# Kernel tuning notes

Hardware: AMD Instinct MI355X
Metric: run time of the kernel (lower is better)

The kernel has to match this reference:

```python
import jax, jax.numpy as jnp
import numpy as np


def _temporal_gated_conv(x, W, b):
    """x: (B,T,N,C) -> (B,T-Kt+1,N,Co). W: (1,Kt,C,2*Co), b: (2*Co,).
    Matches torch Conv2d(in,2*out,(1,Kt)) over (B,C,N,T) followed by GLU."""
    xh = x.transpose(0, 2, 1, 3)  # (B,N,T,C) as NHWC, kernel (1,Kt) over (N,T)
    y = jax.lax.conv_general_dilated(
        xh, W, window_strides=(1, 1), padding='VALID',
        dimension_numbers=('NHWC', 'HWIO', 'NHWC')) + b  # (B,N,T',2Co)
    lhs, rhs = jnp.split(y, 2, axis=-1)
    y = lhs * jax.nn.sigmoid(rhs)
    return y.transpose(0, 2, 1, 3)  # (B,T',N,Co)


def _spatial_graph_conv(x, cheb, Theta):
    """x: (B,T,N,C), cheb: (K,N,N), Theta: (K,C,Co).
    Faithful to torch code: step_x is CUMULATIVELY multiplied by T_k."""
    K = cheb.shape[0]
    cur = x
    acc = jnp.zeros(x.shape[:3] + (Theta.shape[-1],), dtype=x.dtype)
    for k in range(K):  # K is small and structural
        cur = jnp.einsum('mn,btnc->btmc', cheb[k], cur)
        acc = acc + jnp.einsum('btnc,co->btno', cur, Theta[k])
    return jax.nn.relu(acc)


def setup_inputs() -> dict:
    key = jax.random.key(0)
    ks = jax.random.split(key, 7)
    B, T, N, C = 16, 64, 1024, 2
    Kt, Kc, temporal_dim, spatial_dim = 3, 3, 64, 16
    s = 0.05
    return {
        'x': jax.random.normal(ks[0], (B, T, N, C), jnp.float32),
        'cheb': jax.random.normal(ks[1], (Kc, N, N), jnp.float32) * (1.0 / np.sqrt(N)),
        'W1': jax.random.normal(ks[2], (1, Kt, C, 2 * temporal_dim), jnp.float32) * s,
        'b1': jax.random.normal(ks[3], (2 * temporal_dim,), jnp.float32) * s,
        'Theta': jax.random.normal(ks[4], (Kc, temporal_dim, spatial_dim), jnp.float32) * s,
        'W2': jax.random.normal(ks[5], (1, Kt, spatial_dim, 2 * temporal_dim), jnp.float32) * s,
        'b2': jax.random.normal(ks[6], (2 * temporal_dim,), jnp.float32) * s,
    }


def reference(x, cheb, W1, b1, Theta, W2, b2):
    h = _temporal_gated_conv(x, W1, b1)          # (B, T-Kt+1, N, temporal_dim)
    h = _spatial_graph_conv(h, cheb, Theta)      # (B, T-Kt+1, N, spatial_dim)
    out = _temporal_gated_conv(h, W2, b2)        # (B, T-2*(Kt-1), N, temporal_dim)
    return out
```

## Files before the change

### kernel.cpp

```cpp
#include <hip/hip_runtime.h>
#include <stdint.h>

typedef __attribute__((ext_vector_type(8))) short bf16x8;
typedef __attribute__((ext_vector_type(4))) float f32x4;

__device__ __forceinline__ unsigned short f2bf(float f) {
  union { float f; unsigned u; } v; v.f = f;
  unsigned r = v.u + 0x7FFFu + ((v.u >> 16) & 1u);
  return (unsigned short)(r >> 16);
}

__device__ __forceinline__ float sigm(float x) { return 1.0f / (1.0f + __expf(-x)); }

__device__ __forceinline__ void gload16(const void* g, void* l) {
  __builtin_amdgcn_global_load_lds((const __attribute__((address_space(1))) void*)g,
                                   (__attribute__((address_space(3))) void*)l, 16, 0, 0);
}

__device__ __forceinline__ void bar() {
  __builtin_amdgcn_sched_barrier(0);
  __builtin_amdgcn_s_barrier();
  __builtin_amdgcn_sched_barrier(0);
}

__global__ void k0_prep(const float* __restrict__ cheb, unsigned short* __restrict__ cb1,
                        unsigned short* __restrict__ cb2, unsigned short* __restrict__ Pbig) {
  int i = blockIdx.x * blockDim.x + threadIdx.x;
  unsigned short h = f2bf(cheb[i]);
  int which = i >> 20, r = i & 1048575;
  if (which == 0) Pbig[(size_t)(r >> 10) * 3072 + (r & 1023)] = h;
  else if (which == 1) cb1[r] = h;
  else cb2[r] = h;
}

__global__ void tposebf(const unsigned short* __restrict__ s1, int ss1, unsigned short* __restrict__ d1,
                        const unsigned short* __restrict__ s2, int ss2, unsigned short* __restrict__ d2) {
  const unsigned short* src = blockIdx.z ? s2 : s1;
  unsigned short* dst = blockIdx.z ? d2 : d1;
  const int ss = blockIdx.z ? ss2 : ss1;
  __shared__ unsigned short t[64][65];
  const int c = threadIdx.x & 63, r4 = threadIdx.x >> 6;
  const int r0 = blockIdx.y * 64, c0 = blockIdx.x * 64;
#pragma unroll
  for (int r = 0; r < 64; r += 4) t[r + r4][c] = src[(size_t)(r0 + r + r4) * ss + c0 + c];
  __syncthreads();
#pragma unroll
  for (int r = 0; r < 64; r += 4) dst[(size_t)(c0 + r + r4) * 1024 + r0 + c] = t[c][r + r4];
}

__global__ __launch_bounds__(256) void gemm_bt(
    const unsigned short* __restrict__ A, const unsigned short* __restrict__ Bt,
    unsigned short* __restrict__ C, int K, int ldc, int coloff,
    const unsigned short* __restrict__ A2, const unsigned short* __restrict__ Bt2,
    unsigned short* __restrict__ C2, int ldc2, int coloff2) {
  __shared__ __align__(16) unsigned short sA[128 * 32];
  __shared__ __align__(16) unsigned short sB[128 * 32];
  const unsigned short* Ap = A;
  const unsigned short* Bp = Bt;
  unsigned short* Cp = C;
  int ld = ldc, co = coloff;
  if (blockIdx.z) { Ap = A2; Bp = Bt2; Cp = C2; ld = ldc2; co = coloff2; }
  const int mb = blockIdx.x, nb = blockIdx.y;
  const int tid = threadIdx.x;
  const int lane = tid & 63;
  const int w = tid >> 6;
  const int m0 = mb * 128, n0 = nb * 128;
  const int wm = (w >> 1) * 64, wn = (w & 1) * 64;
  const int lr = lane & 15, lg = lane >> 4;
  const f32x4 ZV = {0.f, 0.f, 0.f, 0.f};
  f32x4 acc[4][4];
#pragma unroll
  for (int f = 0; f < 4; ++f)
#pragma unroll
    for (int g = 0; g < 4; ++g) acc[f][g] = ZV;
  const int r2 = tid >> 2, kp = tid & 3;
  const size_t rowA0 = (size_t)(m0 + r2) * K;
  const size_t rowA1 = (size_t)(m0 + 64 + r2) * K;
  const size_t rowB0 = (size_t)(n0 + r2) * K;
  const size_t rowB1 = (size_t)(n0 + 64 + r2) * K;
  unsigned short* la = &sA[w * 512];
  unsigned short* lb = &sB[w * 512];
  for (int k0 = 0; k0 < K; k0 += 32) {
    const int kc = k0 + kp * 8;
    gload16(Ap + rowA0 + kc, la);
    gload16(Ap + rowA1 + kc, la + 2048);
    gload16(Bp + rowB0 + kc, lb);
    gload16(Bp + rowB1 + kc, lb + 2048);
    __syncthreads();
    bf16x8 av[4], bv[4];
#pragma unroll
    for (int f = 0; f < 4; ++f)
      av[f] = *(const bf16x8*)&sA[(wm + f * 16 + lr) * 32 + lg * 8];
#pragma unroll
    for (int g = 0; g < 4; ++g)
      bv[g] = *(const bf16x8*)&sB[(wn + g * 16 + lr) * 32 + lg * 8];
#pragma unroll
    for (int f = 0; f < 4; ++f)
#pragma unroll
      for (int g = 0; g < 4; ++g)
        acc[f][g] = __builtin_amdgcn_mfma_f32_16x16x32_bf16(av[f], bv[g], acc[f][g], 0, 0, 0);
    __syncthreads();
  }
#pragma unroll
  for (int f = 0; f < 4; ++f) {
    const int m = m0 + wm + f * 16 + lg * 4;
#pragma unroll
    for (int g = 0; g < 4; ++g) {
      const int col = co + n0 + wn + g * 16 + lr;
#pragma unroll
      for (int i = 0; i < 4; ++i)
        Cp[(size_t)(m + i) * ld + col] = f2bf(acc[f][g][i]);
    }
  }
}

__device__ __forceinline__ void dec_chunk(int s, int& row, int& c) {
  const int r3 = (((s >> 2) ^ (s >> 4)) & 1) | (((s >> 3) & 1) << 1) | (((s >> 4) & 1) << 2);
  const int u = s ^ r3;
  row = u >> 2;
  c = u & 3;
}

__global__ __launch_bounds__(512, 1) void gemm_big(
    const unsigned short* __restrict__ A, const unsigned short* __restrict__ Bt,
    unsigned short* __restrict__ C) {
  constexpr int K = 3072, NT = 96;
  __shared__ __align__(16) unsigned short lds[3 * 16384];
  const int tid = threadIdx.x;
  const int lane = tid & 63, w = tid >> 6;
  const int wr = w >> 2, wc = w & 3;
  const int lr = lane & 15, lg = lane >> 4;
  const int lin = blockIdx.x;
  const int v = (lin & 7) * 31 + (lin >> 3);
  const int mb = v & 3, nb = v >> 2;
  const int m0 = mb * 256, n0 = nb * 256;

  int r0_, c0_, r1_, c1_;
  dec_chunk((w * 2 + 0) * 64 + lane, r0_, c0_);
  dec_chunk((w * 2 + 1) * 64 + lane, r1_, c1_);
  const unsigned short* sA0 = A + (size_t)(m0 + r0_) * K + c0_ * 8;
  const unsigned short* sA1 = A + (size_t)(m0 + r1_) * K + c1_ * 8;
  const unsigned short* sB0 = Bt + (size_t)(n0 + r0_) * K + c0_ * 8;
  const unsigned short* sB1 = Bt + (size_t)(n0 + r1_) * K + c1_ * 8;
  const int ldsoff0 = (w * 2 + 0) * 512, ldsoff1 = (w * 2 + 1) * 512;

  f32x4 acc[8][4];
  const f32x4 ZV = {0.f, 0.f, 0.f, 0.f};
#pragma unroll
  for (int f = 0; f < 8; ++f)
#pragma unroll
    for (int g = 0; g < 4; ++g) acc[f][g] = ZV;

  const int aoff = (((wr * 128 + lr) * 64 + lg * 16) ^ ((lr & 7) << 4));
  const int boff = (((wc * 64 + lr) * 64 + lg * 16) ^ ((lr & 7) << 4));

#define STAGE(T, BUF)                                          \
  do {                                                         \
    unsigned short* ba_ = lds + (BUF) * 16384;                 \
    const int k0_ = (T) * 32;                                  \
    gload16(sA0 + k0_, ba_ + ldsoff0);                         \
    gload16(sA1 + k0_, ba_ + ldsoff1);                         \
    gload16(sB0 + k0_, ba_ + 8192 + ldsoff0);                  \
    gload16(sB1 + k0_, ba_ + 8192 + ldsoff1);                  \
  } while (0)

  STAGE(0, 0);
  STAGE(1, 1);
  STAGE(2, 2);
  asm volatile("s_waitcnt vmcnt(8)" ::: "memory");
  bar();

  int cur = 0;
  for (int t = 0; t < NT; ++t) {
    {
      const char* ba = (const char*)(lds + cur * 16384);
      const char* bb = ba + 16384;
      bf16x8 av[8], bv[4];
#pragma unroll
      for (int f = 0; f < 8; ++f)
        av[f] = *(const bf16x8*)(ba + aoff + f * 1024);
#pragma unroll
      for (int g = 0; g < 4; ++g)
        bv[g] = *(const bf16x8*)(bb + boff + g * 1024);
      __builtin_amdgcn_s_setprio(1);
#pragma unroll
      for (int f = 0; f < 8; ++f)
#pragma unroll
        for (int g = 0; g < 4; ++g)
          acc[f][g] = __builtin_amdgcn_mfma_f32_16x16x32_bf16(av[f], bv[g], acc[f][g], 0, 0, 0);
      __builtin_amdgcn_s_setprio(0);
    }
    bar();
    if (t + 3 < NT) STAGE(t + 3, cur);
    if (t <= NT - 4) {
      asm volatile("s_waitcnt vmcnt(8)" ::: "memory");
    } else if (t == NT - 3) {
      asm volatile("s_waitcnt vmcnt(4)" ::: "memory");
    } else if (t == NT - 2) {
      asm volatile("s_waitcnt vmcnt(0)" ::: "memory");
    }
    bar();
    cur = (cur == 2) ? 0 : cur + 1;
  }
#undef STAGE

#pragma unroll
  for (int g = 0; g < 4; ++g) {
    const int n = n0 + wc * 64 + g * 16;
    const size_t jb = (size_t)(n >> 4) * 16384;
#pragma unroll
    for (int f = 0; f < 8; ++f) {
      const int m = m0 + wr * 128 + f * 16 + lg * 4;
#pragma unroll
      for (int i = 0; i < 4; ++i)
        C[jb + (size_t)(m + i) * 16 + lr] = f2bf(fmaxf(acc[f][g][i], 0.f));
    }
  }
}

__global__ __launch_bounds__(256) void k1_fused(
    const float* __restrict__ x, const float* __restrict__ W1, const float* __restrict__ b1,
    const float* __restrict__ Theta, unsigned short* __restrict__ Zt) {
  __shared__ __align__(16) unsigned short hs[4 * 64 * 68];
  __shared__ __align__(16) unsigned short th[3 * 16 * 72];
  __shared__ __align__(16) unsigned short tr[64 * 68];
  const int tid = threadIdx.x, lane = tid & 63, w = tid >> 6;
  const int n0 = blockIdx.x * 64;
  const int bt0 = blockIdx.y * 4;
  const int bt = bt0 + w;
  const int b = bt / 62, t = bt - b * 62;
  float xv[6];
#pragma unroll
  for (int kt = 0; kt < 3; ++kt) {
    const float2 p = *(const float2*)&x[(size_t)((b * 64 + t + kt) * 1024 + n0 + lane) * 2];
    xv[kt * 2] = p.x;
    xv[kt * 2 + 1] = p.y;
  }
  float h[64];
#pragma unroll
  for (int ch = 0; ch < 64; ++ch) {
    float l = b1[ch], r = b1[64 + ch];
#pragma unroll
    for (int q = 0; q < 6; ++q) {
      l += xv[q] * W1[q * 128 + ch];
      r += xv[q] * W1[q * 128 + 64 + ch];
    }
    h[ch] = l * sigm(r);
  }
#pragma unroll
  for (int c8 = 0; c8 < 8; ++c8) {
    union { unsigned short u[8]; uint4 v; } pk;
#pragma unroll
    for (int j = 0; j < 8; ++j) pk.u[j] = f2bf(h[c8 * 8 + j]);
    *(uint4*)&hs[(w * 64 + lane) * 68 + c8 * 8] = pk.v;
  }
  for (int idx = tid; idx < 3072; idx += 256) {
    const int kc = idx >> 10, o = (idx >> 6) & 15, c = idx & 63;
    th[kc * 1152 + o * 72 + c] = f2bf(Theta[((kc << 6) | c) * 16 + o]);
  }
  __syncthreads();
  const int lr = lane & 15, lg = lane >> 4;
  const f32x4 ZV = {0.f, 0.f, 0.f, 0.f};
  for (int kc = 0; kc < 3; ++kc) {
    const bf16x8 av0 = *(const bf16x8*)&th[kc * 1152 + lr * 72 + lg * 8];
    const bf16x8 av1 = *(const bf16x8*)&th[kc * 1152 + lr * 72 + 32 + lg * 8];
    f32x4 acc[4];
#pragma unroll
    for (int ns = 0; ns < 4; ++ns) acc[ns] = ZV;
#pragma unroll
    for (int ns = 0; ns < 4; ++ns) {
      const bf16x8 bv0 = *(const bf16x8*)&hs[(w * 64 + ns * 16 + lr) * 68 + lg * 8];
      const bf16x8 bv1 = *(const bf16x8*)&hs[(w * 64 + ns * 16 + lr) * 68 + 32 + lg * 8];
      acc[ns] = __builtin_amdgcn_mfma_f32_16x16x32_bf16(av0, bv0, acc[ns], 0, 0, 0);
      acc[ns] = __builtin_amdgcn_mfma_f32_16x16x32_bf16(av1, bv1, acc[ns], 0, 0, 0);
    }
    if (kc) __syncthreads();
#pragma unroll
    for (int ns = 0; ns < 4; ++ns)
#pragma unroll
      for (int i = 0; i < 4; ++i)
        tr[(w * 16 + lg * 4 + i) * 68 + ns * 16 + lr] = f2bf(acc[ns][i]);
    __syncthreads();
#pragma unroll
    for (int rd = 0; rd < 2; ++rd) {
      const int cidx = rd * 256 + tid;
      const int rl = cidx >> 3, ck = cidx & 7;
      const uint4 v = *(const uint4*)&tr[rl * 68 + ck * 8];
      *(uint4*)&Zt[(size_t)(bt0 * 16 + rl) * 3072 + kc * 1024 + n0 + ck * 8] = v;
    }
  }
}

__global__ __launch_bounds__(256) void k3_out(
    const unsigned short* __restrict__ accb, const float* __restrict__ W2,
    const float* __restrict__ b2, float* __restrict__ out) {
  __shared__ __align__(16) unsigned short sW[128 * 72];
  const int tid = threadIdx.x, lane = tid & 63, w = tid >> 6;
  const int lr = lane & 15, lg = lane >> 4;
  const int n0 = blockIdx.x * 256;
  const int btp = blockIdx.y;
  const int b = btp / 60, tt = btp - b * 60;
  for (int idx = tid; idx < 2048; idx += 256) {
    const int ch = idx >> 4, k = 48 + (idx & 15);
    sW[ch * 72 + k] = 0;
  }
  for (int idx = tid; idx < 6144; idx += 256) {
    const int k = idx >> 7, ch = idx & 127;
    sW[ch * 72 + k] = f2bf(W2[idx]);
  }
  const int rowb = n0 + w * 64;
  const bf16x8 ZB = {0, 0, 0, 0, 0, 0, 0, 0};
  bf16x8 av[4][2];
#pragma unroll
  for (int f = 0; f < 4; ++f)
#pragma unroll
    for (int hh = 0; hh < 2; ++hh) {
      const int gk = hh * 32 + lg * 8;
      const int kt = gk >> 4, ci = gk & 15;
      av[f][hh] = ZB;
      if (kt < 3)
        av[f][hh] = *(const bf16x8*)&accb[(size_t)(b * 62 + tt + kt) * 16384 +
                                          (size_t)(rowb + f * 16 + lr) * 16 + ci];
    }
  __syncthreads();
  const size_t obase = (size_t)(b * 60 + tt) * 65536;
  const f32x4 ZV = {0.f, 0.f, 0.f, 0.f};
#pragma unroll
  for (int gl = 0; gl < 4; ++gl) {
    const int chl = gl * 16 + lr;
    const bf16x8 bl0 = *(const bf16x8*)&sW[chl * 72 + lg * 8];
    const bf16x8 bl1 = *(const bf16x8*)&sW[chl * 72 + 32 + lg * 8];
    const bf16x8 br0 = *(const bf16x8*)&sW[(64 + chl) * 72 + lg * 8];
    const bf16x8 br1 = *(const bf16x8*)&sW[(64 + chl) * 72 + 32 + lg * 8];
    f32x4 aL[4], aR[4];
#pragma unroll
    for (int f = 0; f < 4; ++f) { aL[f] = ZV; aR[f] = ZV; }
#pragma unroll
    for (int f = 0; f < 4; ++f) {
      aL[f] = __builtin_amdgcn_mfma_f32_16x16x32_bf16(av[f][0], bl0, aL[f], 0, 0, 0);
      aL[f] = __builtin_amdgcn_mfma_f32_16x16x32_bf16(av[f][1], bl1, aL[f], 0, 0, 0);
      aR[f] = __builtin_amdgcn_mfma_f32_16x16x32_bf16(av[f][0], br0, aR[f], 0, 0, 0);
      aR[f] = __builtin_amdgcn_mfma_f32_16x16x32_bf16(av[f][1], br1, aR[f], 0, 0, 0);
    }
    const float bbl = b2[chl], bbr = b2[64 + chl];
#pragma unroll
    for (int f = 0; f < 4; ++f)
#pragma unroll
      for (int i = 0; i < 4; ++i) {
        const float pl = aL[f][i] + bbl;
        const float pr = aR[f][i] + bbr;
        out[obase + (size_t)(rowb + f * 16 + lg * 4 + i) * 64 + chl] = pl * sigm(pr);
      }
  }
}

extern "C" void kernel_launch(void* const* d_in, const int* in_sizes, int n_in,
                              void* d_out, int out_size, void* d_ws, size_t ws_size,
                              hipStream_t stream) {
  const float* x    = (const float*)d_in[0];
  const float* cheb = (const float*)d_in[1];
  const float* W1   = (const float*)d_in[2];
  const float* b1   = (const float*)d_in[3];
  const float* Th   = (const float*)d_in[4];
  const float* W2   = (const float*)d_in[5];
  const float* b2   = (const float*)d_in[6];
  float* out = (float*)d_out;

  char* ws = (char*)d_ws;
  const size_t MB = 1u << 20;
  unsigned short* cb1  = (unsigned short*)(ws);
  unsigned short* cb2  = (unsigned short*)(ws + 2 * MB);
  unsigned short* Pbig = (unsigned short*)(ws + 4 * MB);
  unsigned short* t0   = (unsigned short*)(ws + 10 * MB);
  unsigned short* t1   = (unsigned short*)(ws + 12 * MB);
  unsigned short* Qb   = (unsigned short*)(ws + 14 * MB);
  unsigned short* accb = (unsigned short*)(ws + 14 * MB);
  unsigned short* Zt   = (unsigned short*)d_out;

  k0_prep<<<12288, 256, 0, stream>>>(cheb, cb1, cb2, Pbig);
  tposebf<<<dim3(16, 16, 2), 256, 0, stream>>>(Pbig, 3072, t0, cb1, 1024, t1);
  gemm_bt<<<dim3(8, 8, 2), 256, 0, stream>>>(cb1, t0, Pbig, 1024, 3072, 1024,
                                             cb2, t1, Qb, 1024, 0);
  gemm_bt<<<dim3(8, 8, 1), 256, 0, stream>>>(Qb, t0, Pbig, 1024, 3072, 2048,
                                             cb1, t0, Pbig, 1024, 0);
  k1_fused<<<dim3(16, 248), 256, 0, stream>>>(x, W1, b1, Th, Zt);
  gemm_big<<<dim3(248), dim3(512), 0, stream>>>(Pbig, Zt, accb);
  k3_out<<<dim3(4, 960), 256, 0, stream>>>(accb, W2, b2, out);
}
```

Before: 304.0 us.

## Software-pipeline LDS reads with register double-buffering and four-stage global prefetch

Restructures the big GEMM main loop so the LDS fragment reads for the next K-step are issued before the MFMA block of the current step, using two register buffers and a loop unrolled by two. The LDS ring grows from three to four stages, giving one more prefetch in flight. The intent is to hide LDS read latency behind the MFMAs and cut the stall before each barrier. The cost is higher register pressure from the doubled fragments and 128KB of LDS per block. The launch-bounds hint of two blocks per CU likely cannot be met with that much LDS and may just constrain register allocation.

```diff
diff --git a/kernel.cpp b/kernel.cpp
--- a/kernel.cpp
+++ b/kernel.cpp
@@ -121,11 +121,11 @@
   c = u & 3;
 }
 
-__global__ __launch_bounds__(512, 1) void gemm_big(
+__global__ __launch_bounds__(512, 2) void gemm_big(
     const unsigned short* __restrict__ A, const unsigned short* __restrict__ Bt,
     unsigned short* __restrict__ C) {
   constexpr int K = 3072, NT = 96;
-  __shared__ __align__(16) unsigned short lds[3 * 16384];
+  __shared__ __align__(16) unsigned short lds[4 * 16384];
   const int tid = threadIdx.x;
   const int lane = tid & 63, w = tid >> 6;
   const int wr = w >> 2, wc = w & 3;
@@ -154,9 +154,11 @@
   const int aoff = (((wr * 128 + lr) * 64 + lg * 16) ^ ((lr & 7) << 4));
   const int boff = (((wc * 64 + lr) * 64 + lg * 16) ^ ((lr & 7) << 4));
 
-#define STAGE(T, BUF)                                          \
+  bf16x8 avA[8], bvA[4], avB[8], bvB[4];
+
+#define STAGE(T)                                               \
   do {                                                         \
-    unsigned short* ba_ = lds + (BUF) * 16384;                 \
+    unsigned short* ba_ = lds + ((T) & 3) * 16384;             \
     const int k0_ = (T) * 32;                                  \
     gload16(sA0 + k0_, ba_ + ldsoff0);                         \
     gload16(sA1 + k0_, ba_ + ldsoff1);                         \
@@ -164,45 +166,57 @@
     gload16(sB1 + k0_, ba_ + 8192 + ldsoff1);                  \
   } while (0)
 
-  STAGE(0, 0);
-  STAGE(1, 1);
-  STAGE(2, 2);
+#define DSREAD(T, AN, BN)                                      \
+  do {                                                         \
+    const char* rb_ = (const char*)lds + ((T) & 3) * 32768;    \
+    _Pragma("unroll") for (int f_ = 0; f_ < 8; ++f_)           \
+      AN[f_] = *(const bf16x8*)(rb_ + aoff + f_ * 1024);       \
+    _Pragma("unroll") for (int g_ = 0; g_ < 4; ++g_)           \
+      BN[g_] = *(const bf16x8*)(rb_ + 16384 + boff + g_ * 1024); \
+  } while (0)
+
+#define MFMAC(AC, BC)                                          \
+  do {                                                         \
+    __builtin_amdgcn_s_setprio(1);                             \
+    _Pragma("unroll") for (int f_ = 0; f_ < 8; ++f_)           \
+      _Pragma("unroll") for (int g_ = 0; g_ < 4; ++g_)         \
+        acc[f_][g_] = __builtin_amdgcn_mfma_f32_16x16x32_bf16(AC[f_], BC[g_], acc[f_][g_], 0, 0, 0); \
+    __builtin_amdgcn_s_setprio(0);                             \
+  } while (0)
+
+  STAGE(0); STAGE(1); STAGE(2); STAGE(3);
   asm volatile("s_waitcnt vmcnt(8)" ::: "memory");
   bar();
-
-  int cur = 0;
-  for (int t = 0; t < NT; ++t) {
-    {
-      const char* ba = (const char*)(lds + cur * 16384);
-      const char* bb = ba + 16384;
-      bf16x8 av[8], bv[4];
-#pragma unroll
-      for (int f = 0; f < 8; ++f)
-        av[f] = *(const bf16x8*)(ba + aoff + f * 1024);
-#pragma unroll
-      for (int g = 0; g < 4; ++g)
-        bv[g] = *(const bf16x8*)(bb + boff + g * 1024);
-      __builtin_amdgcn_s_setprio(1);
-#pragma unroll
-      for (int f = 0; f < 8; ++f)
-#pragma unroll
-        for (int g = 0; g < 4; ++g)
-          acc[f][g] = __builtin_amdgcn_mfma_f32_16x16x32_bf16(av[f], bv[g], acc[f][g], 0, 0, 0);
-      __builtin_amdgcn_s_setprio(0);
-    }
+  DSREAD(0, avA, bvA);
+
+  for (int tt = 0; tt < NT - 4; tt += 2) {
+    DSREAD(tt + 1, avB, bvB);
+    STAGE(tt + 4);
+    MFMAC(avA, bvA);
+    asm volatile("s_waitcnt vmcnt(8) lgkmcnt(0)" ::: "memory");
     bar();
-    if (t + 3 < NT) STAGE(t + 3, cur);
-    if (t <= NT - 4) {
-      asm volatile("s_waitcnt vmcnt(8)" ::: "memory");
-    } else if (t == NT - 3) {
-      asm volatile("s_waitcnt vmcnt(4)" ::: "memory");
-    } else if (t == NT - 2) {
-      asm volatile("s_waitcnt vmcnt(0)" ::: "memory");
-    }
+    DSREAD(tt + 2, avA, bvA);
+    STAGE(tt + 5);
+    MFMAC(avB, bvB);
+    asm volatile("s_waitcnt vmcnt(8) lgkmcnt(0)" ::: "memory");
     bar();
-    cur = (cur == 2) ? 0 : cur + 1;
-  }
+  }
+  DSREAD(93, avB, bvB);
+  MFMAC(avA, bvA);
+  asm volatile("s_waitcnt vmcnt(4) lgkmcnt(0)" ::: "memory");
+  bar();
+  DSREAD(94, avA, bvA);
+  MFMAC(avB, bvB);
+  asm volatile("s_waitcnt vmcnt(0) lgkmcnt(0)" ::: "memory");
+  bar();
+  DSREAD(95, avB, bvB);
+  MFMAC(avA, bvA);
+  asm volatile("s_waitcnt lgkmcnt(0)" ::: "memory");
+  __builtin_amdgcn_sched_barrier(0);
+  MFMAC(avB, bvB);
 #undef STAGE
+#undef DSREAD
+#undef MFMAC
 
 #pragma unroll
   for (int g = 0; g < 4; ++g) {
```

Result: faster. 296.9 us (-2.3%).
